# Kernel tuning notes

Hardware: AMD Instinct MI355X
Metric: run time of the kernel (lower is better)

The kernel has to match this reference:

```python
import jax, jax.numpy as jnp
import numpy as np

SQRT_2_OVER_PI = 0.7978845608028654

def _gelu_tanh(m):
    inner = SQRT_2_OVER_PI * (m + 0.044715 * m * m * m)
    return 0.5 * m * (1.0 + jnp.tanh(inner))

def setup_inputs() -> dict:
    key = jax.random.key(0)
    k1, k2, k3, k4 = jax.random.split(key, 4)
    M, N, O = 16384, 4096, 16384
    x = jax.random.normal(k1, (M, N), dtype=jnp.float32)
    weight = jax.random.normal(k2, (O, N), dtype=jnp.float32)
    bias = jax.random.normal(k3, (O,), dtype=jnp.float32)
    subtract = jax.random.normal(k4, (O,), dtype=jnp.float32)
    return {"x": x, "weight": weight, "bias": bias, "subtract": subtract, "out_features": O}

def reference(x, weight, bias, subtract, out_features):
    # Parameter-only precompute (recompute_cache): c_i = sum_j W[j,i],
    # col_sum_bias = sum_j (bias_j - subtract_j)
    c = weight.sum(axis=0)                     # [N]
    col_sum_bias = (bias - subtract).sum()     # scalar
    # Per-row collapsed Linear -> subtract -> mean (logsumexp over 1 elem = identity)
    row_sum = x @ c + col_sum_bias             # [M]
    m = row_sum / out_features                 # [M]
    g = _gelu_tanh(m)                          # [M]
    return x + g[:, None]                      # residual broadcast over features
```

## Files before the change

kernel.cpp:

```cpp
#include <hip/hip_runtime.h>
#include <math.h>

#define THREADS 256
#define CHUNKS 512

typedef int v4i __attribute__((ext_vector_type(4)));

__device__ __forceinline__ float4 ntload4(const float* p) {
    v4i t = __builtin_nontemporal_load(reinterpret_cast<const v4i*>(p));
    float4 r;
    r.x = __int_as_float(t.x); r.y = __int_as_float(t.y);
    r.z = __int_as_float(t.z); r.w = __int_as_float(t.w);
    return r;
}
__device__ __forceinline__ void ntstore4(float* p, const float4 v) {
    v4i t;
    t.x = __float_as_int(v.x); t.y = __float_as_int(v.y);
    t.z = __float_as_int(v.z); t.w = __float_as_int(v.w);
    __builtin_nontemporal_store(t, reinterpret_cast<v4i*>(p));
}

__device__ __forceinline__ float gelu_fast(float m) {
    const float inner = 0.7978845608028654f * (m + 0.044715f * m * m * m);
    return m / (1.0f + __expf(-2.0f * inner));
}

__global__ __launch_bounds__(THREADS)
void colsum_partials_kernel(const float* __restrict__ W, float* __restrict__ partials,
                            int O, int N, int rows_per_chunk) {
    int col = (blockIdx.x * THREADS + threadIdx.x) * 4;
    if (col >= N) return;
    int r0 = blockIdx.y * rows_per_chunk;
    int r1 = r0 + rows_per_chunk; if (r1 > O) r1 = O;
    float ax = 0.f, ay = 0.f, az = 0.f, aw = 0.f;
    #pragma unroll 4
    for (int r = r0; r < r1; ++r) {
        const float4 v = ntload4(W + (size_t)r * N + col);
        ax += v.x; ay += v.y; az += v.z; aw += v.w;
    }
    *reinterpret_cast<float4*>(partials + (size_t)blockIdx.y * N + col) =
        make_float4(ax, ay, az, aw);
}

__global__ __launch_bounds__(THREADS)
void reduce_par_kernel(const float* __restrict__ partials,
                       const float* __restrict__ bias, const float* __restrict__ sub,
                       float* __restrict__ c, float* __restrict__ cb,
                       int N, int O, int chunks) {
    const int ncolg = N >> 2;
    const int t = threadIdx.x;
    if ((int)blockIdx.x == ncolg) {
        float s = 0.f;
        for (int i = t; i < O; i += THREADS) s += bias[i] - sub[i];
        #pragma unroll
        for (int off = 32; off > 0; off >>= 1) s += __shfl_down(s, off, 64);
        __shared__ float lds[THREADS / 64];
        if ((t & 63) == 0) lds[t >> 6] = s;
        __syncthreads();
        if (t == 0) {
            float tt = 0.f;
            #pragma unroll
            for (int w = 0; w < THREADS / 64; ++w) tt += lds[w];
            *cb = tt;
        }
        return;
    }
    const int colg = blockIdx.x << 2;
    float ax = 0.f, ay = 0.f, az = 0.f, aw = 0.f;
    for (int k = t; k < chunks; k += THREADS) {
        const float4 v = *reinterpret_cast<const float4*>(partials + (size_t)k * N + colg);
        ax += v.x; ay += v.y; az += v.z; aw += v.w;
    }
    #pragma unroll
    for (int off = 32; off > 0; off >>= 1) {
        ax += __shfl_down(ax, off, 64);
        ay += __shfl_down(ay, off, 64);
        az += __shfl_down(az, off, 64);
        aw += __shfl_down(aw, off, 64);
    }
    __shared__ float4 lds4[THREADS / 64];
    if ((t & 63) == 0) lds4[t >> 6] = make_float4(ax, ay, az, aw);
    __syncthreads();
    if (t == 0) {
        float4 r = lds4[0];
        #pragma unroll
        for (int w = 1; w < THREADS / 64; ++w) {
            r.x += lds4[w].x; r.y += lds4[w].y; r.z += lds4[w].z; r.w += lds4[w].w;
        }
        *reinterpret_cast<float4*>(c + colg) = r;
    }
}

template<int VPL>
__global__ __launch_bounds__(THREADS)
void row_wave_kernel(const float* __restrict__ x, const float* __restrict__ c,
                     const float* __restrict__ cb, const int* __restrict__ of_ptr,
                     float* __restrict__ out, int M, int N) {
    const int wave = threadIdx.x >> 6;
    const int lane = threadIdx.x & 63;
    const int row = blockIdx.x * (THREADS / 64) + wave;
    if (row >= M) return;
    const size_t base = (size_t)row * N;

    float4 xv[VPL];
    float partial = 0.f;
    #pragma unroll
    for (int k = 0; k < VPL; ++k) {
        const int idx = (k * 64 + lane) * 4;
        const float4 xx = *reinterpret_cast<const float4*>(x + base + idx);
        const float4 cc = *reinterpret_cast<const float4*>(c + idx);
        xv[k] = xx;
        partial += xx.x * cc.x + xx.y * cc.y + xx.z * cc.z + xx.w * cc.w;
    }

    #pragma unroll
    for (int off = 1; off < 64; off <<= 1) partial += __shfl_xor(partial, off, 64);

    const float g = gelu_fast((partial + *cb) / (float)(*of_ptr));

    #pragma unroll
    for (int k = 0; k < VPL; ++k) {
        const int idx = (k * 64 + lane) * 4;
        const float4 xx = xv[k];
        ntstore4(out + base + idx, make_float4(xx.x + g, xx.y + g, xx.z + g, xx.w + g));
    }
}

__global__ __launch_bounds__(THREADS)
void row_fused_generic_kernel(const float* __restrict__ x, const float* __restrict__ c,
                              const float* __restrict__ cb, const int* __restrict__ of_ptr,
                              float* __restrict__ out, int N) {
    const size_t base = (size_t)blockIdx.x * N;
    float partial = 0.f;
    for (int i = threadIdx.x; i < N; i += THREADS) partial += x[base + i] * c[i];
    #pragma unroll
    for (int off = 32; off > 0; off >>= 1) partial += __shfl_down(partial, off, 64);
    __shared__ float lds[THREADS / 64];
    if ((threadIdx.x & 63) == 0) lds[threadIdx.x >> 6] = partial;
    __syncthreads();
    float rs = *cb;
    #pragma unroll
    for (int w = 0; w < THREADS / 64; ++w) rs += lds[w];
    const float g = gelu_fast(rs / (float)(*of_ptr));
    for (int i = threadIdx.x; i < N; i += THREADS) out[base + i] = x[base + i] + g;
}

extern "C" void kernel_launch(void* const* d_in, const int* in_sizes, int n_in,
                              void* d_out, int out_size, void* d_ws, size_t ws_size,
                              hipStream_t stream) {
    const float* x    = (const float*)d_in[0];
    const float* W    = (const float*)d_in[1];
    const float* bias = (const float*)d_in[2];
    const float* sub  = (const float*)d_in[3];
    const int* of_ptr = (const int*)d_in[4];

    const int O = in_sizes[2];
    const int N = (int)((long long)in_sizes[1] / O);
    const int M = (int)((long long)in_sizes[0] / N);

    float* ws = (float*)d_ws;
    float* c  = ws;
    float* cb = ws + N;
    float* partials = ws + N + 64;

    const int colblocks = (N + THREADS * 4 - 1) / (THREADS * 4);

    int chunks = CHUNKS;
    {
        long long maxChunks = ((long long)(ws_size / sizeof(float)) - N - 64) / N;
        while (chunks > maxChunks && chunks > 8) chunks >>= 1;
    }
    const int rows_per_chunk = (O + chunks - 1) / chunks;

    dim3 g1(colblocks, chunks);
    colsum_partials_kernel<<<g1, THREADS, 0, stream>>>(W, partials, O, N, rows_per_chunk);

    reduce_par_kernel<<<(N >> 2) + 1, THREADS, 0, stream>>>(
        partials, bias, sub, c, cb, N, O, chunks);

    const int waves_per_block = THREADS / 64;
    const int G = (M + waves_per_block - 1) / waves_per_block;
    if (N == 4096) {
        row_wave_kernel<16><<<G, THREADS, 0, stream>>>(x, c, cb, of_ptr, (float*)d_out, M, N);
    } else if (N == 2048) {
        row_wave_kernel<8><<<G, THREADS, 0, stream>>>(x, c, cb, of_ptr, (float*)d_out, M, N);
    } else if (N == 8192) {
        row_wave_kernel<32><<<G, THREADS, 0, stream>>>(x, c, cb, of_ptr, (float*)d_out, M, N);
    } else {
        row_fused_generic_kernel<<<M, THREADS, 0, stream>>>(x, c, cb, of_ptr, (float*)d_out, N);
    }
}
```

Before: 165.3 us.

## Split row pass into rowsum-GELU kernel and reverse-order broadcast add kernel

For N=4096 the fused single-pass row kernel is replaced by two kernels. The first computes each row's dot product with the column sums and stores the GELU value to workspace. The second re-reads x in reverse order and adds the per-row value, so the tail of x still in the large last-level cache is reused first. This reads x twice instead of once, trading extra traffic for hoped-for cache hits and better streaming; the N=2048/8192 fused paths also swap which side uses nontemporal access.

New measurement: 202.9 us. 1.23x slower.

```diff
diff --git a/kernel.cpp b/kernel.cpp
--- a/kernel.cpp
+++ b/kernel.cpp
@@ -93,6 +93,42 @@
 
 template<int VPL>
 __global__ __launch_bounds__(THREADS)
+void rowsum_gelu_kernel(const float* __restrict__ x, const float* __restrict__ c,
+                        const float* __restrict__ cb, const int* __restrict__ of_ptr,
+                        float* __restrict__ g, int M, int N) {
+    const int wave = threadIdx.x >> 6;
+    const int lane = threadIdx.x & 63;
+    const int row = blockIdx.x * (THREADS / 64) + wave;
+    if (row >= M) return;
+    const size_t base = (size_t)row * N;
+
+    float partial = 0.f;
+    #pragma unroll
+    for (int k = 0; k < VPL; ++k) {
+        const int idx = (k * 64 + lane) * 4;
+        const float4 xx = *reinterpret_cast<const float4*>(x + base + idx);
+        const float4 cc = *reinterpret_cast<const float4*>(c + idx);
+        partial += xx.x * cc.x + xx.y * cc.y + xx.z * cc.z + xx.w * cc.w;
+    }
+    #pragma unroll
+    for (int off = 1; off < 64; off <<= 1) partial += __shfl_xor(partial, off, 64);
+    if (lane == 0) g[row] = gelu_fast((partial + *cb) / (float)(*of_ptr));
+}
+
+__global__ __launch_bounds__(THREADS)
+void addg_kernel(const float* __restrict__ x, const float* __restrict__ g,
+                 float* __restrict__ out, long long n4, int shift) {
+    const long long stride = (long long)gridDim.x * THREADS;
+    for (long long i = (long long)blockIdx.x * THREADS + threadIdx.x; i < n4; i += stride) {
+        const long long j = n4 - 1 - i;
+        const float4 xx = *reinterpret_cast<const float4*>(x + 4 * j);
+        const float gg = g[j >> shift];
+        ntstore4(out + 4 * j, make_float4(xx.x + gg, xx.y + gg, xx.z + gg, xx.w + gg));
+    }
+}
+
+template<int VPL>
+__global__ __launch_bounds__(THREADS)
 void row_wave_kernel(const float* __restrict__ x, const float* __restrict__ c,
                      const float* __restrict__ cb, const int* __restrict__ of_ptr,
                      float* __restrict__ out, int M, int N) {
@@ -101,28 +137,25 @@
     const int row = blockIdx.x * (THREADS / 64) + wave;
     if (row >= M) return;
     const size_t base = (size_t)row * N;
-
     float4 xv[VPL];
     float partial = 0.f;
     #pragma unroll
     for (int k = 0; k < VPL; ++k) {
         const int idx = (k * 64 + lane) * 4;
-        const float4 xx = *reinterpret_cast<const float4*>(x + base + idx);
+        const float4 xx = ntload4(x + base + idx);
         const float4 cc = *reinterpret_cast<const float4*>(c + idx);
         xv[k] = xx;
         partial += xx.x * cc.x + xx.y * cc.y + xx.z * cc.z + xx.w * cc.w;
     }
-
     #pragma unroll
     for (int off = 1; off < 64; off <<= 1) partial += __shfl_xor(partial, off, 64);
-
     const float g = gelu_fast((partial + *cb) / (float)(*of_ptr));
-
     #pragma unroll
     for (int k = 0; k < VPL; ++k) {
         const int idx = (k * 64 + lane) * 4;
         const float4 xx = xv[k];
-        ntstore4(out + base + idx, make_float4(xx.x + g, xx.y + g, xx.z + g, xx.w + g));
+        *reinterpret_cast<float4*>(out + base + idx) =
+            make_float4(xx.x + g, xx.y + g, xx.z + g, xx.w + g);
     }
 }
 
@@ -161,13 +194,14 @@
     float* ws = (float*)d_ws;
     float* c  = ws;
     float* cb = ws + N;
-    float* partials = ws + N + 64;
+    float* g  = ws + N + 64;
+    float* partials = ws + N + 64 + M;
 
     const int colblocks = (N + THREADS * 4 - 1) / (THREADS * 4);
 
     int chunks = CHUNKS;
     {
-        long long maxChunks = ((long long)(ws_size / sizeof(float)) - N - 64) / N;
+        long long maxChunks = ((long long)(ws_size / sizeof(float)) - N - 64 - M) / N;
         while (chunks > maxChunks && chunks > 8) chunks >>= 1;
     }
     const int rows_per_chunk = (O + chunks - 1) / chunks;
@@ -180,11 +214,17 @@
 
     const int waves_per_block = THREADS / 64;
     const int G = (M + waves_per_block - 1) / waves_per_block;
+
+    int shift = 0; { int q = N >> 2; while ((1 << shift) < q) ++shift; }
+    const bool pow2 = ((N & (N - 1)) == 0);
+
     if (N == 4096) {
-        row_wave_kernel<16><<<G, THREADS, 0, stream>>>(x, c, cb, of_ptr, (float*)d_out, M, N);
-    } else if (N == 2048) {
+        rowsum_gelu_kernel<16><<<G, THREADS, 0, stream>>>(x, c, cb, of_ptr, g, M, N);
+        const long long n4 = ((long long)M * N) >> 2;
+        addg_kernel<<<2048, THREADS, 0, stream>>>(x, g, (float*)d_out, n4, shift);
+    } else if (N == 2048 && pow2) {
         row_wave_kernel<8><<<G, THREADS, 0, stream>>>(x, c, cb, of_ptr, (float*)d_out, M, N);
-    } else if (N == 8192) {
+    } else if (N == 8192 && pow2) {
         row_wave_kernel<32><<<G, THREADS, 0, stream>>>(x, c, cb, of_ptr, (float*)d_out, M, N);
     } else {
         row_fused_generic_kernel<<<M, THREADS, 0, stream>>>(x, c, cb, of_ptr, (float*)d_out, N);
```
